# Kernel optimization log

Hardware: AMD Instinct MI355X
Metric: run time of the kernel (lower is better)

The kernel has to match this reference:

```python
import jax, jax.numpy as jnp
import numpy as np

B, M, N = 16, 1024, 4096
CIN, HID = 67, 128  # in_channels+3, hid_channels
BN_EPS = 1e-5


def setup_inputs() -> dict:
    key = jax.random.key(0)
    ks = jax.random.split(key, 13)
    inp = {
        "cent_feat": jax.random.normal(ks[0], (B, M, CIN), dtype=jnp.float32),
        "feat": jax.random.normal(ks[1], (B, N, CIN), dtype=jnp.float32),
        "mask": jax.random.uniform(ks[2], (B, M, N), dtype=jnp.float32),
        # Conv1d(k=1, bias=False) weights, xavier-normal-ish scale
        "Wq": jax.random.normal(ks[3], (HID, CIN), dtype=jnp.float32) * np.float32(np.sqrt(2.0 / (HID + CIN))),
        "Wk": jax.random.normal(ks[4], (HID, CIN), dtype=jnp.float32) * np.float32(np.sqrt(2.0 / (HID + CIN))),
        # BatchNorm1d params (inference form)
        "gq": jax.random.uniform(ks[5], (HID,), dtype=jnp.float32, minval=0.5, maxval=1.5),
        "bq": jax.random.normal(ks[6], (HID,), dtype=jnp.float32) * 0.1,
        "mq": jax.random.normal(ks[7], (HID,), dtype=jnp.float32) * 0.1,
        "vq": jax.random.uniform(ks[8], (HID,), dtype=jnp.float32, minval=0.5, maxval=1.5),
        "gk": jax.random.uniform(ks[9], (HID,), dtype=jnp.float32, minval=0.5, maxval=1.5),
        "bk": jax.random.normal(ks[10], (HID,), dtype=jnp.float32) * 0.1,
        "mk": jax.random.normal(ks[11], (HID,), dtype=jnp.float32) * 0.1,
        "vk": jax.random.uniform(ks[12], (HID,), dtype=jnp.float32, minval=0.5, maxval=1.5),
    }
    return inp


def _bn(x, g, b, m, v):
    # BatchNorm1d over channel dim (last axis here), inference form
    return (x - m) * (g / jnp.sqrt(v + BN_EPS)) + b


def _l1_normalize(x, axis):
    # torch F.normalize(p=1): x / max(||x||_1, 1e-12)
    return x / jnp.maximum(jnp.sum(jnp.abs(x), axis=axis, keepdims=True), 1e-12)


def reference(cent_feat, feat, mask, Wq, Wk, gq, bq, mq, vq, gk, bk, mk, vk):
    # Conv1x1 (1x1 conv = channel matmul) + BN, no activation
    q = _bn(jnp.einsum("bmc,hc->bmh", cent_feat, Wq), gq, bq, mq, vq)  # [B,M,H]
    k = _bn(jnp.einsum("bnc,hc->bnh", feat, Wk), gk, bk, mk, vk)       # [B,N,H]
    adj = jnp.einsum("bmh,bnh->bmn", q, k)                              # [B,M,N]
    adj = jnp.where(mask < 1e-9, jnp.float32(-1e9), adj)
    adj = jax.nn.softmax(adj, axis=-1)
    adj = jnp.sqrt(mask + 1e-9) * jnp.sqrt(adj + 1e-9) - 1e-9
    adj = _l1_normalize(adj, axis=1)
    adj = _l1_normalize(adj, axis=-1)
    return adj
```

## Files before the change

kernel.cpp:

```cpp
#include <hip/hip_runtime.h>
#include <hip/hip_fp16.h>

#define B_ 16
#define M_ 1024
#define N_ 4096
#define H_ 128
#define CIN_ 67

typedef _Float16 half8 __attribute__((ext_vector_type(8)));
typedef _Float16 half4_t __attribute__((ext_vector_type(4)));
typedef float f32x4 __attribute__((ext_vector_type(4)));

#define SPA 104

__global__ __launch_bounds__(256) void k_embed(
    const float* __restrict__ cent, const float* __restrict__ feat,
    const float* __restrict__ Wq, const float* __restrict__ Wk,
    const float* __restrict__ gq, const float* __restrict__ bq,
    const float* __restrict__ mq, const float* __restrict__ vq,
    const float* __restrict__ gk, const float* __restrict__ bk,
    const float* __restrict__ mk, const float* __restrict__ vk,
    __half* __restrict__ q16, __half* __restrict__ k16)
{
  __shared__ __align__(16) __half al[128 * SPA];
  __shared__ __align__(16) __half wl[128 * SPA];
  __shared__ float scl[128], shl[128];

  const int tid = threadIdx.x;
  const int wg  = blockIdx.x;
  const bool isq = (wg < 128);
  const int row0 = isq ? wg * 128 : (wg - 128) * 128;
  const float* in = isq ? cent : feat;
  const float* W  = isq ? Wq : Wk;
  const float* g  = isq ? gq : gk;
  const float* bb = isq ? bq : bk;
  const float* mm = isq ? mq : mk;
  const float* vv = isq ? vq : vk;
  __half* outp = isq ? q16 : k16;

  for (int i = tid; i < 128 * 29; i += 256) {
    int r = i / 29, c = 67 + (i - r * 29);
    al[r * SPA + c] = __float2half(0.f);
    wl[r * SPA + c] = __float2half(0.f);
  }
  for (int i = tid; i < 128 * CIN_; i += 256) {
    int r = i / CIN_, c = i - r * CIN_;
    al[r * SPA + c] = __float2half(in[(size_t)row0 * CIN_ + i]);
    wl[r * SPA + c] = __float2half(W[i]);
  }
  if (tid < 128) {
    float s = g[tid] * rsqrtf(vv[tid] + 1e-5f);
    float sc = isq ? 1.44269504088896f : 1.f;
    scl[tid] = s * sc;
    shl[tid] = (bb[tid] - mm[tid] * s) * sc;
  }
  __syncthreads();

  const int lane = tid & 63, wv = tid >> 6;
  const int col = lane & 15, quad = lane >> 4;

  f32x4 acc[2][8];
#pragma unroll
  for (int ms = 0; ms < 2; ++ms)
#pragma unroll
    for (int ns = 0; ns < 8; ++ns) acc[ms][ns] = (f32x4){0.f, 0.f, 0.f, 0.f};

#pragma unroll
  for (int kk = 0; kk < 3; ++kk) {
    half8 af[2], bf[8];
#pragma unroll
    for (int ms = 0; ms < 2; ++ms)
      af[ms] = *(const half8*)&al[(wv * 32 + ms * 16 + col) * SPA + kk * 32 + quad * 8];
#pragma unroll
    for (int ns = 0; ns < 8; ++ns)
      bf[ns] = *(const half8*)&wl[(ns * 16 + col) * SPA + kk * 32 + quad * 8];
#pragma unroll
    for (int ms = 0; ms < 2; ++ms)
#pragma unroll
      for (int ns = 0; ns < 8; ++ns)
        acc[ms][ns] = __builtin_amdgcn_mfma_f32_16x16x32_f16(af[ms], bf[ns], acc[ms][ns], 0, 0, 0);
  }

#pragma unroll
  for (int ms = 0; ms < 2; ++ms)
#pragma unroll
    for (int reg = 0; reg < 4; ++reg) {
      int r = wv * 32 + ms * 16 + quad * 4 + reg;
#pragma unroll
      for (int ns = 0; ns < 8; ++ns) {
        int h = ns * 16 + col;
        float v = acc[ms][ns][reg] * scl[h] + shl[h];
        outp[(size_t)(row0 + r) * H_ + h] = __float2half(v);
      }
    }
}

#define SPB 136

__global__ __launch_bounds__(256, 4) void k_attn1(
    const __half* __restrict__ q16, const __half* __restrict__ k16,
    float* __restrict__ Z)
{
  __shared__ __align__(16) __half ka[128 * SPB];

  const int tid = threadIdx.x;
  const int b = blockIdx.z, mt = blockIdx.y, ns = blockIdx.x;
  const int m0 = mt * 128;
  const int lane = tid & 63, wv = tid >> 6;
  const int col = lane & 15, quad = lane >> 4;

  const __half* kstrip = k16 + ((size_t)(b * N_) + ns * 512) * H_;

  {
    uint4 kr[8];
    const uint4* s0 = (const uint4*)kstrip;
#pragma unroll
    for (int j = 0; j < 8; ++j) kr[j] = s0[tid + 256 * j];
#pragma unroll
    for (int j = 0; j < 8; ++j) {
      int i = tid + 256 * j;
      *(uint4*)&ka[(i >> 4) * SPB + (i & 15) * 8] = kr[j];
    }
  }
  half8 qf[4][2];
  {
    const __half* qb = q16 + ((size_t)(b * M_) + m0 + wv * 32 + col) * H_;
#pragma unroll
    for (int kk = 0; kk < 4; ++kk)
#pragma unroll
      for (int ms = 0; ms < 2; ++ms)
        qf[kk][ms] = *(const half8*)(qb + (size_t)ms * 16 * H_ + kk * 32 + quad * 8);
  }
  __syncthreads();

  float zacc[8];
#pragma unroll
  for (int i = 0; i < 8; ++i) zacc[i] = 0.f;

  for (int t = 0; t < 4; ++t) {
    f32x4 acc[2][8];
#pragma unroll
    for (int ms = 0; ms < 2; ++ms)
#pragma unroll
      for (int nb = 0; nb < 8; ++nb) acc[ms][nb] = (f32x4){0.f, 0.f, 0.f, 0.f};

#pragma unroll
    for (int kk = 0; kk < 4; ++kk) {
#pragma unroll
      for (int nb = 0; nb < 8; ++nb) {
        half8 bf = *(const half8*)&ka[(nb * 16 + col) * SPB + kk * 32 + quad * 8];
        acc[0][nb] = __builtin_amdgcn_mfma_f32_16x16x32_f16(qf[kk][0], bf, acc[0][nb], 0, 0, 0);
        acc[1][nb] = __builtin_amdgcn_mfma_f32_16x16x32_f16(qf[kk][1], bf, acc[1][nb], 0, 0, 0);
      }
    }

    const uint4* sn = (const uint4*)(kstrip + (size_t)(t + 1) * 128 * H_);
    uint4 kr2[4];
    if (t < 3) {
      __syncthreads();
#pragma unroll
      for (int j = 0; j < 4; ++j) kr2[j] = sn[tid + 256 * j];
    }

#pragma unroll
    for (int reg = 0; reg < 4; ++reg) {
      float s = 0.f;
#pragma unroll
      for (int nb = 0; nb < 8; ++nb) s += exp2f(acc[0][nb][reg]);
      zacc[reg] += s;
    }

    if (t < 3) {
#pragma unroll
      for (int j = 0; j < 4; ++j) {
        int i = tid + 256 * j;
        *(uint4*)&ka[(i >> 4) * SPB + (i & 15) * 8] = kr2[j];
      }
#pragma unroll
      for (int j = 0; j < 4; ++j) kr2[j] = sn[tid + 256 * (j + 4)];
    }

#pragma unroll
    for (int reg = 0; reg < 4; ++reg) {
      float s = 0.f;
#pragma unroll
      for (int nb = 0; nb < 8; ++nb) s += exp2f(acc[1][nb][reg]);
      zacc[4 + reg] += s;
    }

    if (t < 3) {
#pragma unroll
      for (int j = 0; j < 4; ++j) {
        int i = tid + 256 * (j + 4);
        *(uint4*)&ka[(i >> 4) * SPB + (i & 15) * 8] = kr2[j];
      }
      __syncthreads();
    }
  }

#pragma unroll
  for (int i = 0; i < 8; ++i) {
    zacc[i] += __shfl_xor(zacc[i], 1);
    zacc[i] += __shfl_xor(zacc[i], 2);
    zacc[i] += __shfl_xor(zacc[i], 4);
    zacc[i] += __shfl_xor(zacc[i], 8);
  }
  if (col == 0) {
#pragma unroll
    for (int i = 0; i < 8; ++i) {
      int m = m0 + wv * 32 + (i >> 2) * 16 + quad * 4 + (i & 3);
      atomicAdd(&Z[(size_t)b * M_ + m], zacc[i]);
    }
  }
}

__global__ __launch_bounds__(256, 4) void k_attn3(
    const __half* __restrict__ q16, const __half* __restrict__ k16,
    const float* __restrict__ mask, const float* __restrict__ Z,
    __half* __restrict__ t16, float* __restrict__ colsum)
{
  __shared__ __align__(16) __half qa[128 * SPB];

  const int tid = threadIdx.x;
  const int b = blockIdx.z, mt = blockIdx.y, nt = blockIdx.x;
  const int m0 = mt * 128, n0 = nt * 128;
  const int lane = tid & 63, wv = tid >> 6;
  const int col = lane & 15, quad = lane >> 4;

  {
    uint4 qr[8];
    const uint4* sq = (const uint4*)(q16 + ((size_t)(b * M_) + m0) * H_);
#pragma unroll
    for (int j = 0; j < 8; ++j) qr[j] = sq[tid + 256 * j];
#pragma unroll
    for (int j = 0; j < 8; ++j) {
      int i = tid + 256 * j;
      *(uint4*)&qa[(i >> 4) * SPB + (i & 15) * 8] = qr[j];
    }
  }
  half8 kf[4][2];
  {
    const __half* kb = k16 + ((size_t)(b * N_) + n0 + wv * 32 + col) * H_;
#pragma unroll
    for (int kk = 0; kk < 4; ++kk)
#pragma unroll
      for (int ms = 0; ms < 2; ++ms)
        kf[kk][ms] = *(const half8*)(kb + (size_t)ms * 16 * H_ + kk * 32 + quad * 8);
  }
  __syncthreads();

  f32x4 acc[2][8];
#pragma unroll
  for (int ms = 0; ms < 2; ++ms)
#pragma unroll
    for (int nb = 0; nb < 8; ++nb) acc[ms][nb] = (f32x4){0.f, 0.f, 0.f, 0.f};

#pragma unroll
  for (int kk = 0; kk < 4; ++kk) {
#pragma unroll
    for (int nb = 0; nb < 8; ++nb) {
      half8 bf = *(const half8*)&qa[(nb * 16 + col) * SPB + kk * 32 + quad * 8];
      acc[0][nb] = __builtin_amdgcn_mfma_f32_16x16x32_f16(kf[kk][0], bf, acc[0][nb], 0, 0, 0);
      acc[1][nb] = __builtin_amdgcn_mfma_f32_16x16x32_f16(kf[kk][1], bf, acc[1][nb], 0, 0, 0);
    }
  }
  __syncthreads();

  float lz[8];
#pragma unroll
  for (int nsm = 0; nsm < 8; ++nsm)
    lz[nsm] = __log2f(Z[(size_t)b * M_ + m0 + nsm * 16 + col]);

  float cs[8];
#pragma unroll
  for (int i = 0; i < 8; ++i) cs[i] = 0.f;

#pragma unroll
  for (int msN = 0; msN < 2; ++msN) {
    const int nl = wv * 32 + msN * 16 + quad * 4;
#pragma unroll
    for (int nsm = 0; nsm < 8; ++nsm) {
      const int ml = nsm * 16 + col;
      const float lzv = lz[nsm];
      const float4 mv = *(const float4*)&mask[((size_t)b * M_ + m0 + ml) * N_ + n0 + nl];
      half4_t h;
#pragma unroll
      for (int reg = 0; reg < 4; ++reg) {
        float mvv = (reg == 0) ? mv.x : (reg == 1) ? mv.y : (reg == 2) ? mv.z : mv.w;
        float x = acc[msN][nsm][reg];
        x = (mvv < 1e-9f) ? -1e9f : x;
        float p = exp2f(x - lzv);
        float t = sqrtf((mvv + 1e-9f) * (p + 1e-9f)) - 1e-9f;
        h[reg] = (_Float16)t;
        cs[msN * 4 + reg] += t;
      }
      *(half4_t*)&qa[ml * SPB + nl] = h;
    }
  }
  __syncthreads();

#pragma unroll
  for (int j = 0; j < 8; ++j) {
    int i = tid + 256 * j;
    int r = i >> 4, u = i & 15;
    *(uint4*)&t16[((size_t)(b * M_) + m0 + r) * N_ + n0 + u * 8] =
        *(const uint4*)&qa[r * SPB + u * 8];
  }

#pragma unroll
  for (int i = 0; i < 8; ++i) {
    cs[i] += __shfl_xor(cs[i], 1);
    cs[i] += __shfl_xor(cs[i], 2);
    cs[i] += __shfl_xor(cs[i], 4);
    cs[i] += __shfl_xor(cs[i], 8);
  }
  if (col == 0) {
#pragma unroll
    for (int i = 0; i < 8; ++i) {
      int n = n0 + wv * 32 + (i >> 2) * 16 + quad * 4 + (i & 3);
      atomicAdd(&colsum[(size_t)b * N_ + n], cs[i]);
    }
  }
}

__global__ __launch_bounds__(256) void k_icol(float* __restrict__ cs)
{
  int i = blockIdx.x * 256 + threadIdx.x;
  cs[i] = 1.f / fmaxf(cs[i], 1e-12f);
}

__global__ __launch_bounds__(256) void k_norm(
    const __half* __restrict__ t16, float* __restrict__ out,
    const float* __restrict__ icol)
{
  const int row = blockIdx.x;
  const int b = row >> 10;
  const half4_t* t4 = (const half4_t*)(t16 + (size_t)row * N_);
  float4* o4 = (float4*)(out + (size_t)row * N_);
  const float4* c4 = (const float4*)(icol + (size_t)b * N_);
  const int tid = threadIdx.x;

  float4 u[4];
  float s = 0.f;
#pragma unroll
  for (int j = 0; j < 4; ++j) {
    int idx = tid + 256 * j;
    half4_t h = t4[idx];
    float4 c = c4[idx];
    u[j].x = (float)h[0] * c.x;
    u[j].y = (float)h[1] * c.y;
    u[j].z = (float)h[2] * c.z;
    u[j].w = (float)h[3] * c.w;
    s += u[j].x + u[j].y + u[j].z + u[j].w;
  }
  s += __shfl_xor(s, 1);
  s += __shfl_xor(s, 2);
  s += __shfl_xor(s, 4);
  s += __shfl_xor(s, 8);
  s += __shfl_xor(s, 16);
  s += __shfl_xor(s, 32);
  __shared__ float red[4];
  if ((tid & 63) == 0) red[tid >> 6] = s;
  __syncthreads();
  float tot = red[0] + red[1] + red[2] + red[3];
  float inv = 1.f / fmaxf(tot, 1e-12f);
#pragma unroll
  for (int j = 0; j < 4; ++j) {
    int idx = tid + 256 * j;
    float4 v = u[j];
    v.x *= inv; v.y *= inv; v.z *= inv; v.w *= inv;
    o4[idx] = v;
  }
}

extern "C" void kernel_launch(void* const* d_in, const int* in_sizes, int n_in,
                              void* d_out, int out_size, void* d_ws, size_t ws_size,
                              hipStream_t stream) {
  const float* cent = (const float*)d_in[0];
  const float* feat = (const float*)d_in[1];
  const float* mask = (const float*)d_in[2];
  const float* Wq = (const float*)d_in[3];
  const float* Wk = (const float*)d_in[4];
  const float* gq = (const float*)d_in[5];
  const float* bq = (const float*)d_in[6];
  const float* mq = (const float*)d_in[7];
  const float* vq = (const float*)d_in[8];
  const float* gk = (const float*)d_in[9];
  const float* bk = (const float*)d_in[10];
  const float* mk = (const float*)d_in[11];
  const float* vk = (const float*)d_in[12];
  float* out = (float*)d_out;

  char* ws = (char*)d_ws;
  __half* q16  = (__half*)(ws + 0);
  __half* k16  = (__half*)(ws + 4194304);
  __half* t16  = (__half*)(ws + 20971520);
  float* colsum= (float*)(ws + 155189248);
  float* Zr    = (float*)(ws + 155451392);

  hipMemsetAsync(colsum, 0, 262144 + 65536, stream);

  k_embed<<<640, 256, 0, stream>>>(cent, feat, Wq, Wk, gq, bq, mq, vq,
                                   gk, bk, mk, vk, q16, k16);

  dim3 g1(8, 8, 16);
  k_attn1<<<g1, 256, 0, stream>>>(q16, k16, Zr);

  dim3 g3(N_ / 128, M_ / 128, B_);
  k_attn3<<<g3, 256, 0, stream>>>(q16, k16, mask, Zr, t16, colsum);
  k_icol<<<B_ * N_ / 256, 256, 0, stream>>>(colsum);
  k_norm<<<B_ * M_, 256, 0, stream>>>(t16, out, colsum);
}
```

Baseline: 618.4 us.

## Halve attn3 M tile, XOR-swizzle LDS, and prefetch mask before epilogue barrier

Shrinks the k_attn3 tile from 128 to 64 M rows, doubling the grid and raising the occupancy hint to 5 blocks per CU. It replaces the padded LDS layout with an XOR-swizzled unpadded one to avoid bank conflicts. It also issues all mask and Z loads right after the MFMA loop, pinned with asm barriers, so their global latency overlaps the sync. The trade-off is twice as many colsum atomics and K-fragment loads per output element, in exchange for better latency hiding on the dominant mask stream.

```diff
diff --git a/kernel.cpp b/kernel.cpp
--- a/kernel.cpp
+++ b/kernel.cpp
@@ -214,28 +214,29 @@
   }
 }
 
-__global__ __launch_bounds__(256, 4) void k_attn3(
+__global__ __launch_bounds__(256, 5) void k_attn3(
     const __half* __restrict__ q16, const __half* __restrict__ k16,
     const float* __restrict__ mask, const float* __restrict__ Z,
     __half* __restrict__ t16, float* __restrict__ colsum)
 {
-  __shared__ __align__(16) __half qa[128 * SPB];
+  __shared__ __align__(16) __half qa[64 * 128];
 
   const int tid = threadIdx.x;
   const int b = blockIdx.z, mt = blockIdx.y, nt = blockIdx.x;
-  const int m0 = mt * 128, n0 = nt * 128;
+  const int m0 = mt * 64, n0 = nt * 128;
   const int lane = tid & 63, wv = tid >> 6;
   const int col = lane & 15, quad = lane >> 4;
 
   {
-    uint4 qr[8];
+    uint4 qr[4];
     const uint4* sq = (const uint4*)(q16 + ((size_t)(b * M_) + m0) * H_);
 #pragma unroll
-    for (int j = 0; j < 8; ++j) qr[j] = sq[tid + 256 * j];
-#pragma unroll
-    for (int j = 0; j < 8; ++j) {
+    for (int j = 0; j < 4; ++j) qr[j] = sq[tid + 256 * j];
+#pragma unroll
+    for (int j = 0; j < 4; ++j) {
       int i = tid + 256 * j;
-      *(uint4*)&qa[(i >> 4) * SPB + (i & 15) * 8] = qr[j];
+      int r = i >> 4, c = i & 15;
+      *(uint4*)&qa[r * 128 + ((c * 8) ^ ((r & 7) << 3))] = qr[j];
     }
   }
   half8 kf[4][2];
@@ -249,27 +250,48 @@
   }
   __syncthreads();
 
-  f32x4 acc[2][8];
+  f32x4 acc[2][4];
 #pragma unroll
   for (int ms = 0; ms < 2; ++ms)
 #pragma unroll
-    for (int nb = 0; nb < 8; ++nb) acc[ms][nb] = (f32x4){0.f, 0.f, 0.f, 0.f};
+    for (int nb = 0; nb < 4; ++nb) acc[ms][nb] = (f32x4){0.f, 0.f, 0.f, 0.f};
 
 #pragma unroll
   for (int kk = 0; kk < 4; ++kk) {
 #pragma unroll
-    for (int nb = 0; nb < 8; ++nb) {
-      half8 bf = *(const half8*)&qa[(nb * 16 + col) * SPB + kk * 32 + quad * 8];
+    for (int nb = 0; nb < 4; ++nb) {
+      int row = nb * 16 + col;
+      half8 bf = *(const half8*)&qa[row * 128 + ((kk * 32 + quad * 8) ^ ((col & 7) << 3))];
       acc[0][nb] = __builtin_amdgcn_mfma_f32_16x16x32_f16(kf[kk][0], bf, acc[0][nb], 0, 0, 0);
       acc[1][nb] = __builtin_amdgcn_mfma_f32_16x16x32_f16(kf[kk][1], bf, acc[1][nb], 0, 0, 0);
     }
   }
-  __syncthreads();
-
-  float lz[8];
-#pragma unroll
-  for (int nsm = 0; nsm < 8; ++nsm)
-    lz[nsm] = __log2f(Z[(size_t)b * M_ + m0 + nsm * 16 + col]);
+
+  float zr[4];
+#pragma unroll
+  for (int nsm = 0; nsm < 4; ++nsm)
+    zr[nsm] = Z[(size_t)b * M_ + m0 + nsm * 16 + col];
+  float4 mv[8];
+#pragma unroll
+  for (int msN = 0; msN < 2; ++msN) {
+    const int nb = n0 + wv * 32 + msN * 16 + quad * 4;
+#pragma unroll
+    for (int nsm = 0; nsm < 4; ++nsm)
+      mv[msN * 4 + nsm] =
+          *(const float4*)&mask[((size_t)b * M_ + m0 + nsm * 16 + col) * N_ + nb];
+  }
+#pragma unroll
+  for (int i = 0; i < 8; ++i)
+    asm volatile("" : "+v"(mv[i].x), "+v"(mv[i].y), "+v"(mv[i].z), "+v"(mv[i].w));
+#pragma unroll
+  for (int i = 0; i < 4; ++i) asm volatile("" : "+v"(zr[i]));
+  __builtin_amdgcn_sched_barrier(0);
+
+  __syncthreads();
+
+  float lz[4];
+#pragma unroll
+  for (int i = 0; i < 4; ++i) lz[i] = __log2f(zr[i]);
 
   float cs[8];
 #pragma unroll
@@ -279,14 +301,14 @@
   for (int msN = 0; msN < 2; ++msN) {
     const int nl = wv * 32 + msN * 16 + quad * 4;
 #pragma unroll
-    for (int nsm = 0; nsm < 8; ++nsm) {
+    for (int nsm = 0; nsm < 4; ++nsm) {
       const int ml = nsm * 16 + col;
       const float lzv = lz[nsm];
-      const float4 mv = *(const float4*)&mask[((size_t)b * M_ + m0 + ml) * N_ + n0 + nl];
+      const float4 m4 = mv[msN * 4 + nsm];
       half4_t h;
 #pragma unroll
       for (int reg = 0; reg < 4; ++reg) {
-        float mvv = (reg == 0) ? mv.x : (reg == 1) ? mv.y : (reg == 2) ? mv.z : mv.w;
+        float mvv = (reg == 0) ? m4.x : (reg == 1) ? m4.y : (reg == 2) ? m4.z : m4.w;
         float x = acc[msN][nsm][reg];
         x = (mvv < 1e-9f) ? -1e9f : x;
         float p = exp2f(x - lzv);
@@ -294,17 +316,8 @@
         h[reg] = (_Float16)t;
         cs[msN * 4 + reg] += t;
       }
-      *(half4_t*)&qa[ml * SPB + nl] = h;
-    }
-  }
-  __syncthreads();
-
-#pragma unroll
-  for (int j = 0; j < 8; ++j) {
-    int i = tid + 256 * j;
-    int r = i >> 4, u = i & 15;
-    *(uint4*)&t16[((size_t)(b * M_) + m0 + r) * N_ + n0 + u * 8] =
-        *(const uint4*)&qa[r * SPB + u * 8];
+      *(half4_t*)&qa[ml * 128 + (nl ^ ((ml & 7) << 3))] = h;
+    }
   }
 
 #pragma unroll
@@ -314,6 +327,16 @@
     cs[i] += __shfl_xor(cs[i], 4);
     cs[i] += __shfl_xor(cs[i], 8);
   }
+  __syncthreads();
+
+#pragma unroll
+  for (int j = 0; j < 4; ++j) {
+    int i = tid + 256 * j;
+    int r = i >> 4, u = i & 15;
+    *(uint4*)&t16[((size_t)(b * M_) + m0 + r) * N_ + n0 + u * 8] =
+        *(const uint4*)&qa[r * 128 + ((u * 8) ^ ((r & 7) << 3))];
+  }
+
   if (col == 0) {
 #pragma unroll
     for (int i = 0; i < 8; ++i) {
@@ -406,7 +429,7 @@
   dim3 g1(8, 8, 16);
   k_attn1<<<g1, 256, 0, stream>>>(q16, k16, Zr);
 
-  dim3 g3(N_ / 128, M_ / 128, B_);
+  dim3 g3(N_ / 128, M_ / 64, B_);
   k_attn3<<<g3, 256, 0, stream>>>(q16, k16, mask, Zr, t16, colsum);
   k_icol<<<B_ * N_ / 256, 256, 0, stream>>>(colsum);
   k_norm<<<B_ * M_, 256, 0, stream>>>(t16, out, colsum);
```

Result: no change. 607.5 us (-1.8%).

## Compute logits once as int16 fixed-point and split softmax into separate pass

Applied to the files above, without the earlier changes.

Replaces the two-pass recompute of the QK^T GEMM with a single GEMM kernel that stores clamped logits as 16-bit fixed point and accumulates the softmax denominator from them. A new streaming kernel reads the stored logits and mask to produce the sqrt-weighted values and column sums. This removes a redundant matrix multiply but adds a large intermediate write and read, and introduces quantization of the logits.

```diff
diff --git a/kernel.cpp b/kernel.cpp
--- a/kernel.cpp
+++ b/kernel.cpp
@@ -10,6 +10,8 @@
 typedef _Float16 half8 __attribute__((ext_vector_type(8)));
 typedef _Float16 half4_t __attribute__((ext_vector_type(4)));
 typedef float f32x4 __attribute__((ext_vector_type(4)));
+typedef short s16x4 __attribute__((ext_vector_type(4)));
+typedef short s16x8 __attribute__((ext_vector_type(8)));
 
 #define SPA 104
 
@@ -97,127 +99,9 @@
 
 #define SPB 136
 
-__global__ __launch_bounds__(256, 4) void k_attn1(
+__global__ __launch_bounds__(256, 4) void k_logits(
     const __half* __restrict__ q16, const __half* __restrict__ k16,
-    float* __restrict__ Z)
-{
-  __shared__ __align__(16) __half ka[128 * SPB];
-
-  const int tid = threadIdx.x;
-  const int b = blockIdx.z, mt = blockIdx.y, ns = blockIdx.x;
-  const int m0 = mt * 128;
-  const int lane = tid & 63, wv = tid >> 6;
-  const int col = lane & 15, quad = lane >> 4;
-
-  const __half* kstrip = k16 + ((size_t)(b * N_) + ns * 512) * H_;
-
-  {
-    uint4 kr[8];
-    const uint4* s0 = (const uint4*)kstrip;
-#pragma unroll
-    for (int j = 0; j < 8; ++j) kr[j] = s0[tid + 256 * j];
-#pragma unroll
-    for (int j = 0; j < 8; ++j) {
-      int i = tid + 256 * j;
-      *(uint4*)&ka[(i >> 4) * SPB + (i & 15) * 8] = kr[j];
-    }
-  }
-  half8 qf[4][2];
-  {
-    const __half* qb = q16 + ((size_t)(b * M_) + m0 + wv * 32 + col) * H_;
-#pragma unroll
-    for (int kk = 0; kk < 4; ++kk)
-#pragma unroll
-      for (int ms = 0; ms < 2; ++ms)
-        qf[kk][ms] = *(const half8*)(qb + (size_t)ms * 16 * H_ + kk * 32 + quad * 8);
-  }
-  __syncthreads();
-
-  float zacc[8];
-#pragma unroll
-  for (int i = 0; i < 8; ++i) zacc[i] = 0.f;
-
-  for (int t = 0; t < 4; ++t) {
-    f32x4 acc[2][8];
-#pragma unroll
-    for (int ms = 0; ms < 2; ++ms)
-#pragma unroll
-      for (int nb = 0; nb < 8; ++nb) acc[ms][nb] = (f32x4){0.f, 0.f, 0.f, 0.f};
-
-#pragma unroll
-    for (int kk = 0; kk < 4; ++kk) {
-#pragma unroll
-      for (int nb = 0; nb < 8; ++nb) {
-        half8 bf = *(const half8*)&ka[(nb * 16 + col) * SPB + kk * 32 + quad * 8];
-        acc[0][nb] = __builtin_amdgcn_mfma_f32_16x16x32_f16(qf[kk][0], bf, acc[0][nb], 0, 0, 0);
-        acc[1][nb] = __builtin_amdgcn_mfma_f32_16x16x32_f16(qf[kk][1], bf, acc[1][nb], 0, 0, 0);
-      }
-    }
-
-    const uint4* sn = (const uint4*)(kstrip + (size_t)(t + 1) * 128 * H_);
-    uint4 kr2[4];
-    if (t < 3) {
-      __syncthreads();
-#pragma unroll
-      for (int j = 0; j < 4; ++j) kr2[j] = sn[tid + 256 * j];
-    }
-
-#pragma unroll
-    for (int reg = 0; reg < 4; ++reg) {
-      float s = 0.f;
-#pragma unroll
-      for (int nb = 0; nb < 8; ++nb) s += exp2f(acc[0][nb][reg]);
-      zacc[reg] += s;
-    }
-
-    if (t < 3) {
-#pragma unroll
-      for (int j = 0; j < 4; ++j) {
-        int i = tid + 256 * j;
-        *(uint4*)&ka[(i >> 4) * SPB + (i & 15) * 8] = kr2[j];
-      }
-#pragma unroll
-      for (int j = 0; j < 4; ++j) kr2[j] = sn[tid + 256 * (j + 4)];
-    }
-
-#pragma unroll
-    for (int reg = 0; reg < 4; ++reg) {
-      float s = 0.f;
-#pragma unroll
-      for (int nb = 0; nb < 8; ++nb) s += exp2f(acc[1][nb][reg]);
-      zacc[4 + reg] += s;
-    }
-
-    if (t < 3) {
-#pragma unroll
-      for (int j = 0; j < 4; ++j) {
-        int i = tid + 256 * (j + 4);
-        *(uint4*)&ka[(i >> 4) * SPB + (i & 15) * 8] = kr2[j];
-      }
-      __syncthreads();
-    }
-  }
-
-#pragma unroll
-  for (int i = 0; i < 8; ++i) {
-    zacc[i] += __shfl_xor(zacc[i], 1);
-    zacc[i] += __shfl_xor(zacc[i], 2);
-    zacc[i] += __shfl_xor(zacc[i], 4);
-    zacc[i] += __shfl_xor(zacc[i], 8);
-  }
-  if (col == 0) {
-#pragma unroll
-    for (int i = 0; i < 8; ++i) {
-      int m = m0 + wv * 32 + (i >> 2) * 16 + quad * 4 + (i & 3);
-      atomicAdd(&Z[(size_t)b * M_ + m], zacc[i]);
-    }
-  }
-}
-
-__global__ __launch_bounds__(256, 4) void k_attn3(
-    const __half* __restrict__ q16, const __half* __restrict__ k16,
-    const float* __restrict__ mask, const float* __restrict__ Z,
-    __half* __restrict__ t16, float* __restrict__ colsum)
+    short* __restrict__ x16, float* __restrict__ Z)
 {
   __shared__ __align__(16) __half qa[128 * SPB];
 
@@ -266,35 +150,20 @@
   }
   __syncthreads();
 
-  float lz[8];
-#pragma unroll
-  for (int nsm = 0; nsm < 8; ++nsm)
-    lz[nsm] = __log2f(Z[(size_t)b * M_ + m0 + nsm * 16 + col]);
-
-  float cs[8];
-#pragma unroll
-  for (int i = 0; i < 8; ++i) cs[i] = 0.f;
-
+  short* qs = (short*)qa;
 #pragma unroll
   for (int msN = 0; msN < 2; ++msN) {
     const int nl = wv * 32 + msN * 16 + quad * 4;
 #pragma unroll
     for (int nsm = 0; nsm < 8; ++nsm) {
       const int ml = nsm * 16 + col;
-      const float lzv = lz[nsm];
-      const float4 mv = *(const float4*)&mask[((size_t)b * M_ + m0 + ml) * N_ + n0 + nl];
-      half4_t h;
+      s16x4 s4;
 #pragma unroll
       for (int reg = 0; reg < 4; ++reg) {
-        float mvv = (reg == 0) ? mv.x : (reg == 1) ? mv.y : (reg == 2) ? mv.z : mv.w;
-        float x = acc[msN][nsm][reg];
-        x = (mvv < 1e-9f) ? -1e9f : x;
-        float p = exp2f(x - lzv);
-        float t = sqrtf((mvv + 1e-9f) * (p + 1e-9f)) - 1e-9f;
-        h[reg] = (_Float16)t;
-        cs[msN * 4 + reg] += t;
+        float x = fminf(fmaxf(acc[msN][nsm][reg], -126.f), 126.f);
+        s4[reg] = (short)__float2int_rn(x * 256.f);
       }
-      *(half4_t*)&qa[ml * SPB + nl] = h;
+      *(s16x4*)&qs[ml * SPB + nl] = s4;
     }
   }
   __syncthreads();
@@ -303,23 +172,77 @@
   for (int j = 0; j < 8; ++j) {
     int i = tid + 256 * j;
     int r = i >> 4, u = i & 15;
-    *(uint4*)&t16[((size_t)(b * M_) + m0 + r) * N_ + n0 + u * 8] =
-        *(const uint4*)&qa[r * SPB + u * 8];
-  }
-
-#pragma unroll
-  for (int i = 0; i < 8; ++i) {
-    cs[i] += __shfl_xor(cs[i], 1);
-    cs[i] += __shfl_xor(cs[i], 2);
-    cs[i] += __shfl_xor(cs[i], 4);
-    cs[i] += __shfl_xor(cs[i], 8);
-  }
-  if (col == 0) {
-#pragma unroll
-    for (int i = 0; i < 8; ++i) {
-      int n = n0 + wv * 32 + (i >> 2) * 16 + quad * 4 + (i & 3);
-      atomicAdd(&colsum[(size_t)b * N_ + n], cs[i]);
-    }
+    s16x8 v = *(const s16x8*)&qs[r * SPB + u * 8];
+    *(s16x8*)&x16[((size_t)(b * M_) + m0 + r) * N_ + n0 + u * 8] = v;
+    float s = 0.f;
+#pragma unroll
+    for (int c = 0; c < 8; ++c) s += exp2f((float)v[c] * 0.00390625f);
+    s += __shfl_xor(s, 1);
+    s += __shfl_xor(s, 2);
+    s += __shfl_xor(s, 4);
+    s += __shfl_xor(s, 8);
+    if ((tid & 15) == 0) atomicAdd(&Z[(size_t)b * M_ + m0 + r], s);
+  }
+}
+
+__global__ __launch_bounds__(256, 6) void k_t(
+    const short* __restrict__ x16, const float* __restrict__ mask,
+    const float* __restrict__ Z, __half* __restrict__ t16,
+    float* __restrict__ colsum)
+{
+  __shared__ float lzb[256];
+  __shared__ float cb[4][128];
+
+  const int tid = threadIdx.x;
+  const int b = blockIdx.z, msp = blockIdx.y, nt = blockIdx.x;
+  const int m1 = msp * 256, n0 = nt * 128;
+
+  lzb[tid] = __log2f(Z[(size_t)b * M_ + m1 + tid]);
+  __syncthreads();
+
+  const int nlane = tid & 31, msub = tid >> 5;
+  const int n = n0 + nlane * 4;
+
+  float ca[4] = {0.f, 0.f, 0.f, 0.f};
+
+  for (int mo = 0; mo < 32; mo += 4) {
+    float4 mv[4];
+    s16x4 xv[4];
+    size_t bs[4];
+#pragma unroll
+    for (int k = 0; k < 4; ++k) {
+      const int m = m1 + (mo + k) * 8 + msub;
+      bs[k] = ((size_t)b * M_ + m) * N_ + n;
+      mv[k] = *(const float4*)&mask[bs[k]];
+      xv[k] = *(const s16x4*)&x16[bs[k]];
+    }
+#pragma unroll
+    for (int k = 0; k < 4; ++k) {
+      const float lz = lzb[(mo + k) * 8 + msub];
+      half4_t h;
+#pragma unroll
+      for (int c = 0; c < 4; ++c) {
+        float mvv = (c == 0) ? mv[k].x : (c == 1) ? mv[k].y : (c == 2) ? mv[k].z : mv[k].w;
+        float p = (mvv < 1e-9f) ? 0.f : exp2f((float)xv[k][c] * 0.00390625f - lz);
+        float t = sqrtf((mvv + 1e-9f) * (p + 1e-9f)) - 1e-9f;
+        h[c] = (_Float16)t;
+        ca[c] += t;
+      }
+      *(half4_t*)&t16[bs[k]] = h;
+    }
+  }
+
+#pragma unroll
+  for (int c = 0; c < 4; ++c) ca[c] += __shfl_xor(ca[c], 32);
+  const int wv = tid >> 6;
+  if ((tid & 63) < 32) {
+#pragma unroll
+    for (int c = 0; c < 4; ++c) cb[wv][nlane * 4 + c] = ca[c];
+  }
+  __syncthreads();
+  if (tid < 128) {
+    float s = cb[0][tid] + cb[1][tid] + cb[2][tid] + cb[3][tid];
+    atomicAdd(&colsum[(size_t)b * N_ + n0 + tid], s);
   }
 }
 
@@ -394,20 +317,22 @@
   char* ws = (char*)d_ws;
   __half* q16  = (__half*)(ws + 0);
   __half* k16  = (__half*)(ws + 4194304);
-  __half* t16  = (__half*)(ws + 20971520);
-  float* colsum= (float*)(ws + 155189248);
-  float* Zr    = (float*)(ws + 155451392);
+  short* x16   = (short*)(ws + 20971520);
+  __half* t16  = (__half*)(ws + 155189248);
+  float* colsum= (float*)(ws + 289406976);
+  float* Zr    = (float*)(ws + 289669120);
 
   hipMemsetAsync(colsum, 0, 262144 + 65536, stream);
 
   k_embed<<<640, 256, 0, stream>>>(cent, feat, Wq, Wk, gq, bq, mq, vq,
                                    gk, bk, mk, vk, q16, k16);
 
-  dim3 g1(8, 8, 16);
-  k_attn1<<<g1, 256, 0, stream>>>(q16, k16, Zr);
-
-  dim3 g3(N_ / 128, M_ / 128, B_);
-  k_attn3<<<g3, 256, 0, stream>>>(q16, k16, mask, Zr, t16, colsum);
+  dim3 gl(N_ / 128, M_ / 128, B_);
+  k_logits<<<gl, 256, 0, stream>>>(q16, k16, x16, Zr);
+
+  dim3 gt(N_ / 128, M_ / 256, B_);
+  k_t<<<gt, 256, 0, stream>>>(x16, mask, Zr, t16, colsum);
+
   k_icol<<<B_ * N_ / 256, 256, 0, stream>>>(colsum);
   k_norm<<<B_ * M_, 256, 0, stream>>>(t16, out, colsum);
 }
```

Measured after the change: 685.5 us. 10.9% more time.
